# Kernel tuning notes

Measured on AMD Instinct MI355X. Metric: run time of the kernel, lower is better.

## Reference

```python
import jax, jax.numpy as jnp
import numpy as np
from jax.scipy.special import logsumexp

EXPERT_NUM = 64
MOE_TOPK = 2

def setup_inputs() -> dict:
    key = jax.random.key(0)
    k1, k2 = jax.random.split(key)
    x = jax.random.normal(k1, (4, 4096, 4096), dtype=jnp.float32)
    # nn.Linear(input_size, expert_num).weight has shape [expert_num, input_size]
    W = jax.random.normal(k2, (EXPERT_NUM, 4096), dtype=jnp.float32) * (1.0 / np.sqrt(4096))
    return {"x": x, "W": W}

def reference(x, W):
    # logits: [B, S, E]
    logits = jnp.einsum('bsd,ed->bse', x, W)
    k = min(MOE_TOPK + 1, EXPERT_NUM)  # torch takes topk+1 then slices
    topk_logits, topk_indices = jax.lax.top_k(logits, k)
    topk_logits = topk_logits[..., :MOE_TOPK]     # [B, S, K]
    topk_indices = topk_indices[..., :MOE_TOPK]   # [B, S, K]
    # regularized=True: softmax over the top-k logits in float32
    topk_scores = jax.nn.softmax(topk_logits.astype(jnp.float32), axis=-1).astype(logits.dtype)
    # scatter into zeros; topk indices are unique so one-hot sum == scatter-set
    scores_filtered = jnp.sum(
        jax.nn.one_hot(topk_indices, EXPERT_NUM, dtype=logits.dtype) * topk_scores[..., None],
        axis=-2)  # [B, S, E]
    # router_z loss, per-token [B, S]
    log_z = logsumexp(logits, axis=-1)
    loss = log_z ** 2
    return logits, scores_filtered, loss
```

## Files before the change

### kernel.cpp

```cpp
#include <hip/hip_runtime.h>
#include <math.h>

#define TTOK 16384
#define DD   4096
#define EE   64
#define TM   32
#define BK   64
#define NCH  (DD / BK)

typedef __attribute__((ext_vector_type(8))) short short8;
typedef __attribute__((ext_vector_type(4))) float f32x4;

static __device__ __forceinline__ unsigned short f2bf(float f) {
    unsigned u = __float_as_uint(f);
    u += 0x7FFFu + ((u >> 16) & 1u);
    return (unsigned short)(u >> 16);
}
static __device__ __forceinline__ float bf2f(unsigned short h) {
    return __uint_as_float(((unsigned)h) << 16);
}
static __device__ __forceinline__ void cvt8(f32x4 a, f32x4 b, short8& hi, short8& lo) {
    const float v[8] = {a[0], a[1], a[2], a[3], b[0], b[1], b[2], b[3]};
#pragma unroll
    for (int j = 0; j < 8; ++j) {
        const unsigned short h = f2bf(v[j]);
        hi[j] = (short)h;
        lo[j] = (short)f2bf(v[j] - bf2f(h));
    }
}

__global__ void w_convert(const float* __restrict__ W,
                          unsigned short* __restrict__ whi,
                          unsigned short* __restrict__ wlo) {
    const int t   = blockIdx.x * blockDim.x + threadIdx.x;
    const int m   = t & 15;
    const int q   = (t >> 4) & 3;
    const int eg  = (t >> 6) & 3;
    const int kss = (t >> 8) & 1;
    const int kc  = t >> 9;
    const int E   = eg * 16 + m;
    const int k0  = kc * BK + kss * 32 + q * 8;
    const float* src = W + (size_t)E * DD + k0;
    const f32x4 a = *reinterpret_cast<const f32x4*>(src);
    const f32x4 b = *reinterpret_cast<const f32x4*>(src + 4);
    short8 h, l;
    cvt8(a, b, h, l);
    *reinterpret_cast<short8*>(whi + (size_t)t * 8) = h;
    *reinterpret_cast<short8*>(wlo + (size_t)t * 8) = l;
}

__global__ __launch_bounds__(256, 2)
void moe_fused(const float* __restrict__ x,
               const unsigned short* __restrict__ whi,
               const unsigned short* __restrict__ wlo,
               float* __restrict__ out)
{
    __shared__ unsigned short xh[TM * 64];
    __shared__ unsigned short xl[TM * 64];
    __shared__ float lg[TM * 68];

    const int tid  = threadIdx.x;
    const int wv   = tid >> 6;
    const int lane = tid & 63;
    const int m    = lane & 15;
    const int q    = lane >> 4;
    const int tg   = wv >> 1;
    const int eh   = wv & 1;
    const int t0   = blockIdx.x * TM;

    const int sr = tid >> 3;
    const int sj = tid & 7;
    const int xo = sr * 64 + (sj ^ (sr & 7)) * 8;
    const float* gx = x + (size_t)(t0 + sr) * DD + sj * 8;

    const int wb = eh * 1024 + lane * 8;

    f32x4 acc0 = (f32x4){0.f, 0.f, 0.f, 0.f};
    f32x4 acc1 = (f32x4){0.f, 0.f, 0.f, 0.f};

    short8 pA0, pA1, pA2, pA3, pA4, pA5, pA6, pA7;
    short8 pB0, pB1, pB2, pB3, pB4, pB5, pB6, pB7;

    {
        const unsigned short* bh = whi + wb;
        const unsigned short* bl = wlo + wb;
        pA0 = *reinterpret_cast<const short8*>(bh);
        pA1 = *reinterpret_cast<const short8*>(bh + 512);
        pA2 = *reinterpret_cast<const short8*>(bh + 2048);
        pA3 = *reinterpret_cast<const short8*>(bh + 2560);
        pA4 = *reinterpret_cast<const short8*>(bl);
        pA5 = *reinterpret_cast<const short8*>(bl + 512);
        pA6 = *reinterpret_cast<const short8*>(bl + 2048);
        pA7 = *reinterpret_cast<const short8*>(bl + 2560);
    }
    f32x4 fxA0 = __builtin_nontemporal_load(reinterpret_cast<const f32x4*>(gx));
    f32x4 fxA1 = __builtin_nontemporal_load(reinterpret_cast<const f32x4*>(gx + 4));
    f32x4 fxB0 = __builtin_nontemporal_load(reinterpret_cast<const f32x4*>(gx + BK));
    f32x4 fxB1 = __builtin_nontemporal_load(reinterpret_cast<const f32x4*>(gx + BK + 4));

    const int sa = m & 7;
    const int ra = (16 * tg + m) * 64;

#define CHUNK_BODY(KC, FX0, FX1, PC0, PC1, PC2, PC3, PC4, PC5, PC6, PC7,            \
                         PN0, PN1, PN2, PN3, PN4, PN5, PN6, PN7)                    \
    do {                                                                            \
        __builtin_amdgcn_s_barrier();            \
        __builtin_amdgcn_sched_barrier(0);                                          \
        {                         \
            const int kn_ = ((KC) + 1 < NCH) ? (KC) + 1 : NCH - 1;                  \
            const unsigned short* bh_ = whi + (size_t)kn_ * 4096 + wb;              \
            const unsigned short* bl_ = wlo + (size_t)kn_ * 4096 + wb;              \
            PN0 = *reinterpret_cast<const short8*>(bh_);                            \
            PN1 = *reinterpret_cast<const short8*>(bh_ + 512);                      \
            PN2 = *reinterpret_cast<const short8*>(bh_ + 2048);                     \
            PN3 = *reinterpret_cast<const short8*>(bh_ + 2560);                     \
            PN4 = *reinterpret_cast<const short8*>(bl_);                            \
            PN5 = *reinterpret_cast<const short8*>(bl_ + 512);                      \
            PN6 = *reinterpret_cast<const short8*>(bl_ + 2048);                     \
            PN7 = *reinterpret_cast<const short8*>(bl_ + 2560);                     \
        }                                                                           \
        __builtin_amdgcn_sched_barrier(0);                                          \
        {                     \
            short8 h_, l_;                                                          \
            cvt8(FX0, FX1, h_, l_);                                                 \
            *reinterpret_cast<short8*>(xh + xo) = h_;                               \
            *reinterpret_cast<short8*>(xl + xo) = l_;                               \
        }                                                                           \
        {                           \
            const int kf_ = ((KC) + 2 < NCH) ? (KC) + 2 : NCH - 1;                  \
            FX0 = __builtin_nontemporal_load(                                       \
                      reinterpret_cast<const f32x4*>(gx + kf_ * BK));               \
            FX1 = __builtin_nontemporal_load(                                       \
                      reinterpret_cast<const f32x4*>(gx + kf_ * BK + 4));           \
        }                                                                           \
        asm volatile("s_waitcnt lgkmcnt(0)" ::: "memory");   \
        __builtin_amdgcn_s_barrier();                   \
        __builtin_amdgcn_sched_barrier(0);                                          \
        {                            \
            const int ca0 = (q ^ sa) * 8;                                           \
            const int ca1 = ((4 + q) ^ sa) * 8;                                     \
            const short8 ah0 = *reinterpret_cast<const short8*>(xh + ra + ca0);     \
            const short8 al0 = *reinterpret_cast<const short8*>(xl + ra + ca0);     \
            const short8 ah1 = *reinterpret_cast<const short8*>(xh + ra + ca1);     \
            const short8 al1 = *reinterpret_cast<const short8*>(xl + ra + ca1);     \
            acc0 = __builtin_amdgcn_mfma_f32_16x16x32_bf16(ah0, PC0, acc0, 0, 0, 0);\
            acc0 = __builtin_amdgcn_mfma_f32_16x16x32_bf16(ah0, PC4, acc0, 0, 0, 0);\
            acc0 = __builtin_amdgcn_mfma_f32_16x16x32_bf16(al0, PC0, acc0, 0, 0, 0);\
            acc1 = __builtin_amdgcn_mfma_f32_16x16x32_bf16(ah0, PC1, acc1, 0, 0, 0);\
            acc1 = __builtin_amdgcn_mfma_f32_16x16x32_bf16(ah0, PC5, acc1, 0, 0, 0);\
            acc1 = __builtin_amdgcn_mfma_f32_16x16x32_bf16(al0, PC1, acc1, 0, 0, 0);\
            acc0 = __builtin_amdgcn_mfma_f32_16x16x32_bf16(ah1, PC2, acc0, 0, 0, 0);\
            acc0 = __builtin_amdgcn_mfma_f32_16x16x32_bf16(ah1, PC6, acc0, 0, 0, 0);\
            acc0 = __builtin_amdgcn_mfma_f32_16x16x32_bf16(al1, PC2, acc0, 0, 0, 0);\
            acc1 = __builtin_amdgcn_mfma_f32_16x16x32_bf16(ah1, PC3, acc1, 0, 0, 0);\
            acc1 = __builtin_amdgcn_mfma_f32_16x16x32_bf16(ah1, PC7, acc1, 0, 0, 0);\
            acc1 = __builtin_amdgcn_mfma_f32_16x16x32_bf16(al1, PC3, acc1, 0, 0, 0);\
        }                                                                           \
    } while (0)

    for (int kt = 0; kt < NCH / 2; ++kt) {
        const int k0 = 2 * kt;
        CHUNK_BODY(k0,     fxA0, fxA1, pA0, pA1, pA2, pA3, pA4, pA5, pA6, pA7,
                                       pB0, pB1, pB2, pB3, pB4, pB5, pB6, pB7);
        CHUNK_BODY(k0 + 1, fxB0, fxB1, pB0, pB1, pB2, pB3, pB4, pB5, pB6, pB7,
                                       pA0, pA1, pA2, pA3, pA4, pA5, pA6, pA7);
    }
#undef CHUNK_BODY

    {
        float* lr = lg + (16 * tg + 4 * q) * 68 + 32 * eh + m;
#pragma unroll
        for (int i = 0; i < 4; ++i) {
            lr[i * 68]      = acc0[i];
            lr[i * 68 + 16] = acc1[i];
        }
    }
    __syncthreads();

    const int tt = tid >> 3;
    const int jj = tid & 7;
    const float* row = lg + tt * 68 + jj * 8;
    const f32x4 lv0 = *reinterpret_cast<const f32x4*>(row);
    const f32x4 lv1 = *reinterpret_cast<const f32x4*>(row + 4);
    const float r[8] = {lv0[0], lv0[1], lv0[2], lv0[3], lv1[0], lv1[1], lv1[2], lv1[3]};

    float* gout = out + (size_t)(t0 + tt) * EE + jj * 8;
    *reinterpret_cast<f32x4*>(gout)     = lv0;
    *reinterpret_cast<f32x4*>(gout + 4) = lv1;

    float v1 = -INFINITY, v2 = -INFINITY;
    int   i1 = 0, i2 = 0;
#pragma unroll
    for (int c = 0; c < 8; ++c) {
        const int e = jj * 8 + c;
        const float v = r[c];
        if (v > v1)      { v2 = v1; i2 = i1; v1 = v; i1 = e; }
        else if (v > v2) { v2 = v;  i2 = e; }
    }
#pragma unroll
    for (int mk = 1; mk < 8; mk <<= 1) {
        const float ov1 = __shfl_xor(v1, mk);
        const int   oi1 = __shfl_xor(i1, mk);
        const float ov2 = __shfl_xor(v2, mk);
        const int   oi2 = __shfl_xor(i2, mk);
        const bool aw = (v1 > ov1) || (v1 == ov1 && i1 < oi1);
        const float c1v = aw ? v1 : ov1;  const int c1i = aw ? i1 : oi1;
        const float cav = aw ? v2 : ov2;  const int cai = aw ? i2 : oi2;
        const float cbv = aw ? ov1 : v1;  const int cbi = aw ? oi1 : i1;
        const bool bw = (cav > cbv) || (cav == cbv && cai < cbi);
        v1 = c1v; i1 = c1i;
        v2 = bw ? cav : cbv;
        i2 = bw ? cai : cbi;
    }

    float sm = 0.f;
#pragma unroll
    for (int c = 0; c < 8; ++c) sm += expf(r[c] - v1);
#pragma unroll
    for (int mk = 1; mk < 8; mk <<= 1) sm += __shfl_xor(sm, mk);

    const float logz = v1 + logf(sm);
    if (jj == 0) out[(size_t)2 * TTOK * EE + t0 + tt] = logz * logz;

    const float e21 = expf(v2 - v1);
    const float rr  = 1.f / (1.f + e21);
    const float sc1 = rr, sc2 = e21 * rr;
    float* sc = out + (size_t)TTOK * EE + (size_t)(t0 + tt) * EE + jj * 8;
    float vv[8];
#pragma unroll
    for (int c = 0; c < 8; ++c) {
        const int e = jj * 8 + c;
        vv[c] = (e == i1) ? sc1 : ((e == i2) ? sc2 : 0.f);
    }
    *reinterpret_cast<f32x4*>(sc)     = (f32x4){vv[0], vv[1], vv[2], vv[3]};
    *reinterpret_cast<f32x4*>(sc + 4) = (f32x4){vv[4], vv[5], vv[6], vv[7]};
}

extern "C" void kernel_launch(void* const* d_in, const int* in_sizes, int n_in,
                              void* d_out, int out_size, void* d_ws, size_t ws_size,
                              hipStream_t stream) {
    const float* x = (const float*)d_in[0];
    const float* W = (const float*)d_in[1];
    float* out = (float*)d_out;
    unsigned short* whi = (unsigned short*)d_ws;
    unsigned short* wlo = whi + (size_t)EE * DD;

    w_convert<<<dim3(EE * DD / 8 / 256), dim3(256), 0, stream>>>(W, whi, wlo);
    moe_fused<<<dim3(TTOK / TM), dim3(256), 0, stream>>>(x, whi, wlo, out);
}
```

Before: 377.8 us.

## Double-buffer x tile in LDS to remove one barrier per chunk

Splits the shared-memory bf16 hi/lo x tiles into two buffers and stages chunk k+1 into one buffer while MFMAs read chunk k from the other. This removes the second barrier per chunk, leaving one barrier per step, so more LDS writes and global prefetch can overlap with the MFMA work. It also prefetches x one chunk further ahead, which costs more LDS and live registers and may reduce occupancy.

```diff
diff --git a/kernel.cpp b/kernel.cpp
--- a/kernel.cpp
+++ b/kernel.cpp
@@ -55,8 +55,8 @@
                const unsigned short* __restrict__ wlo,
                float* __restrict__ out)
 {
-    __shared__ unsigned short xh[TM * 64];
-    __shared__ unsigned short xl[TM * 64];
+    __shared__ unsigned short xh[2][TM * 64];
+    __shared__ unsigned short xl[2][TM * 64];
     __shared__ float lg[TM * 68];
 
     const int tid  = threadIdx.x;
@@ -93,20 +93,28 @@
         pA6 = *reinterpret_cast<const short8*>(bl + 2048);
         pA7 = *reinterpret_cast<const short8*>(bl + 2560);
     }
-    f32x4 fxA0 = __builtin_nontemporal_load(reinterpret_cast<const f32x4*>(gx));
-    f32x4 fxA1 = __builtin_nontemporal_load(reinterpret_cast<const f32x4*>(gx + 4));
-    f32x4 fxB0 = __builtin_nontemporal_load(reinterpret_cast<const f32x4*>(gx + BK));
-    f32x4 fxB1 = __builtin_nontemporal_load(reinterpret_cast<const f32x4*>(gx + BK + 4));
+    f32x4 fxE0 = __builtin_nontemporal_load(reinterpret_cast<const f32x4*>(gx));
+    f32x4 fxE1 = __builtin_nontemporal_load(reinterpret_cast<const f32x4*>(gx + 4));
+    f32x4 fxO0 = __builtin_nontemporal_load(reinterpret_cast<const f32x4*>(gx + BK));
+    f32x4 fxO1 = __builtin_nontemporal_load(reinterpret_cast<const f32x4*>(gx + BK + 4));
+    {
+        short8 h0, l0;
+        cvt8(fxE0, fxE1, h0, l0);
+        *reinterpret_cast<short8*>(&xh[0][xo]) = h0;
+        *reinterpret_cast<short8*>(&xl[0][xo]) = l0;
+        fxE0 = __builtin_nontemporal_load(reinterpret_cast<const f32x4*>(gx + 2 * BK));
+        fxE1 = __builtin_nontemporal_load(reinterpret_cast<const f32x4*>(gx + 2 * BK + 4));
+    }
+    asm volatile("s_waitcnt lgkmcnt(0)" ::: "memory");
+    __builtin_amdgcn_s_barrier();
 
     const int sa = m & 7;
     const int ra = (16 * tg + m) * 64;
 
-#define CHUNK_BODY(KC, FX0, FX1, PC0, PC1, PC2, PC3, PC4, PC5, PC6, PC7,            \
-                         PN0, PN1, PN2, PN3, PN4, PN5, PN6, PN7)                    \
+#define CHUNK_BODY(KC, WB, RB, FX0, FX1, PC0, PC1, PC2, PC3, PC4, PC5, PC6, PC7,    \
+                                 PN0, PN1, PN2, PN3, PN4, PN5, PN6, PN7)            \
     do {                                                                            \
-        __builtin_amdgcn_s_barrier();            \
-        __builtin_amdgcn_sched_barrier(0);                                          \
-        {                         \
+        {        \
             const int kn_ = ((KC) + 1 < NCH) ? (KC) + 1 : NCH - 1;                  \
             const unsigned short* bh_ = whi + (size_t)kn_ * 4096 + wb;              \
             const unsigned short* bl_ = wlo + (size_t)kn_ * 4096 + wb;              \
@@ -120,29 +128,26 @@
             PN7 = *reinterpret_cast<const short8*>(bl_ + 2560);                     \
         }                                                                           \
         __builtin_amdgcn_sched_barrier(0);                                          \
-        {                     \
+        {         \
             short8 h_, l_;                                                          \
             cvt8(FX0, FX1, h_, l_);                                                 \
-            *reinterpret_cast<short8*>(xh + xo) = h_;                               \
-            *reinterpret_cast<short8*>(xl + xo) = l_;                               \
-        }                                                                           \
-        {                           \
-            const int kf_ = ((KC) + 2 < NCH) ? (KC) + 2 : NCH - 1;                  \
+            *reinterpret_cast<short8*>(&xh[WB][xo]) = h_;                           \
+            *reinterpret_cast<short8*>(&xl[WB][xo]) = l_;                           \
+        }                                                                           \
+        {                                 \
+            const int kf_ = ((KC) + 3 < NCH) ? (KC) + 3 : NCH - 1;                  \
             FX0 = __builtin_nontemporal_load(                                       \
                       reinterpret_cast<const f32x4*>(gx + kf_ * BK));               \
             FX1 = __builtin_nontemporal_load(                                       \
                       reinterpret_cast<const f32x4*>(gx + kf_ * BK + 4));           \
         }                                                                           \
-        asm volatile("s_waitcnt lgkmcnt(0)" ::: "memory");   \
-        __builtin_amdgcn_s_barrier();                   \
-        __builtin_amdgcn_sched_barrier(0);                                          \
-        {                            \
+        {                         \
             const int ca0 = (q ^ sa) * 8;                                           \
             const int ca1 = ((4 + q) ^ sa) * 8;                                     \
-            const short8 ah0 = *reinterpret_cast<const short8*>(xh + ra + ca0);     \
-            const short8 al0 = *reinterpret_cast<const short8*>(xl + ra + ca0);     \
-            const short8 ah1 = *reinterpret_cast<const short8*>(xh + ra + ca1);     \
-            const short8 al1 = *reinterpret_cast<const short8*>(xl + ra + ca1);     \
+            const short8 ah0 = *reinterpret_cast<const short8*>(&xh[RB][ra + ca0]); \
+            const short8 al0 = *reinterpret_cast<const short8*>(&xl[RB][ra + ca0]); \
+            const short8 ah1 = *reinterpret_cast<const short8*>(&xh[RB][ra + ca1]); \
+            const short8 al1 = *reinterpret_cast<const short8*>(&xl[RB][ra + ca1]); \
             acc0 = __builtin_amdgcn_mfma_f32_16x16x32_bf16(ah0, PC0, acc0, 0, 0, 0);\
             acc0 = __builtin_amdgcn_mfma_f32_16x16x32_bf16(ah0, PC4, acc0, 0, 0, 0);\
             acc0 = __builtin_amdgcn_mfma_f32_16x16x32_bf16(al0, PC0, acc0, 0, 0, 0);\
@@ -156,14 +161,16 @@
             acc1 = __builtin_amdgcn_mfma_f32_16x16x32_bf16(ah1, PC7, acc1, 0, 0, 0);\
             acc1 = __builtin_amdgcn_mfma_f32_16x16x32_bf16(al1, PC3, acc1, 0, 0, 0);\
         }                                                                           \
+        asm volatile("s_waitcnt lgkmcnt(0)" ::: "memory");      \
+        __builtin_amdgcn_s_barrier();             \
     } while (0)
 
     for (int kt = 0; kt < NCH / 2; ++kt) {
         const int k0 = 2 * kt;
-        CHUNK_BODY(k0,     fxA0, fxA1, pA0, pA1, pA2, pA3, pA4, pA5, pA6, pA7,
-                                       pB0, pB1, pB2, pB3, pB4, pB5, pB6, pB7);
-        CHUNK_BODY(k0 + 1, fxB0, fxB1, pB0, pB1, pB2, pB3, pB4, pB5, pB6, pB7,
-                                       pA0, pA1, pA2, pA3, pA4, pA5, pA6, pA7);
+        CHUNK_BODY(k0,     1, 0, fxO0, fxO1, pA0, pA1, pA2, pA3, pA4, pA5, pA6, pA7,
+                                             pB0, pB1, pB2, pB3, pB4, pB5, pB6, pB7);
+        CHUNK_BODY(k0 + 1, 0, 1, fxE0, fxE1, pB0, pB1, pB2, pB3, pB4, pB5, pB6, pB7,
+                                             pA0, pA1, pA2, pA3, pA4, pA5, pA6, pA7);
     }
 #undef CHUNK_BODY
 
```

Result: no change. 377.2 us (-0.1%).
